# Performance work log

Measured on AMD Instinct MI355X. Metric: run time of the kernel, lower is better.

## Reference

```python
import jax, jax.numpy as jnp
import numpy as np

HIDDEN = 128
INPUT_DIM = 1
NUM_CLASSES = 2


def setup_inputs() -> dict:
    key = jax.random.key(0)
    ks = jax.random.split(key, 7)
    B, T = 256, 1024
    s_ih = 1.0 / np.sqrt(HIDDEN)
    x = jax.random.normal(ks[0], (B, T, INPUT_DIM), dtype=jnp.float32)
    W_ih = jax.random.uniform(ks[1], (HIDDEN, INPUT_DIM), jnp.float32, -s_ih, s_ih)
    W_hh = jax.random.uniform(ks[2], (HIDDEN, HIDDEN), jnp.float32, -s_ih, s_ih)
    b_ih = jax.random.uniform(ks[3], (HIDDEN,), jnp.float32, -s_ih, s_ih)
    b_hh = jax.random.uniform(ks[4], (HIDDEN,), jnp.float32, -s_ih, s_ih)
    W_fc = jax.random.uniform(ks[5], (NUM_CLASSES, HIDDEN), jnp.float32, -s_ih, s_ih)
    b_fc = jax.random.uniform(ks[6], (NUM_CLASSES,), jnp.float32, -s_ih, s_ih)
    return {"x": x, "W_ih": W_ih, "W_hh": W_hh, "b_ih": b_ih,
            "b_hh": b_hh, "W_fc": W_fc, "b_fc": b_fc}


def reference(x, W_ih, W_hh, b_ih, b_hh, W_fc, b_fc):
    B = x.shape[0]
    # Precompute input projection for all timesteps: [B,T,H]
    xp = jnp.einsum('bti,hi->bth', x, W_ih) + b_ih + b_hh
    h0 = jnp.zeros((B, HIDDEN), dtype=x.dtype)

    def step(h, xp_t):
        h_new = jnp.tanh(xp_t + h @ W_hh.T)  # [B,H]
        return h_new, h_new

    _, hs = jax.lax.scan(step, h0, jnp.swapaxes(xp, 0, 1))  # hs: [T,B,H]
    out = jnp.swapaxes(hs, 0, 1)  # [B,T,H]
    logits = jnp.einsum('bth,ch->btc', out, W_fc) + b_fc  # [B,T,C]
    return logits
```

## Files before the change

### kernel.cpp

```cpp
#include <hip/hip_runtime.h>

typedef float f32x2 __attribute__((ext_vector_type(2)));
typedef float f32x4 __attribute__((ext_vector_type(4)));

#define BB 256
#define TT 1024
#define HH 128
#define CC 2

#define LOG2E2 2.885390081777927f

__device__ __forceinline__ float ftanh2(float u2) {
    float e = __builtin_amdgcn_exp2f(u2);
    float r = __builtin_amdgcn_rcpf(e + 1.0f);
    return fmaf(-2.0f, r, 1.0f);
}

__device__ __forceinline__ float bcast(float v, int j) {
    return __int_as_float(__builtin_amdgcn_readlane(__float_as_int(v), j));
}

#define DPP_ADD(v, ctrl)                                                     \
    ((v) + __int_as_float(__builtin_amdgcn_mov_dpp(                          \
         __float_as_int(v), (ctrl), 0xF, 0xF, true)))

#define SYNC() asm volatile("s_waitcnt lgkmcnt(0)\n\ts_barrier" ::: "memory")

__global__ __launch_bounds__(256, 1) void rnn_kernel(
    const float* __restrict__ x, const float* __restrict__ W_ih,
    const float* __restrict__ W_hh, const float* __restrict__ b_ih,
    const float* __restrict__ b_hh, const float* __restrict__ W_fc,
    const float* __restrict__ b_fc, float* __restrict__ out)
{
    const int b   = blockIdx.x;
    const int tid = threadIdx.x;
    const int l   = tid & 63;
    const int wv  = tid >> 6;
    const int lq  = l & 31;
    const int kb  = wv << 5;
    const int rA  = l, rB = l + 64;
    const int rF  = kb + lq;

    __shared__ float xs[TT + 8];
    __shared__ f32x2 p2[2][4][64];
    __shared__ f32x2 qp[4][4];
    __shared__ f32x2 obuf[16];

    {
        const f32x4* xr = (const f32x4*)(x + (size_t)b * TT);
        ((f32x4*)xs)[tid] = xr[tid];
    }
    if (tid < 8) xs[TT + tid] = 0.f;

    const float wih  = W_ih[rF] * LOG2E2;
    const float bias = (b_ih[rF] + b_hh[rF]) * LOG2E2;
    const float wfs  = (l < 32) ? W_fc[rF] : W_fc[HH + rF];
    const float bf0  = b_fc[0], bf1 = b_fc[1];

    float wa[32], wb[32];
    {
        const f32x4* a4 = (const f32x4*)(W_hh + (size_t)rA * HH + kb);
        const f32x4* b4 = (const f32x4*)(W_hh + (size_t)rB * HH + kb);
        #pragma unroll
        for (int j = 0; j < 8; ++j) {
            f32x4 va = a4[j], vb = b4[j];
            wa[4*j+0] = va.x * LOG2E2; wa[4*j+1] = va.y * LOG2E2;
            wa[4*j+2] = va.z * LOG2E2; wa[4*j+3] = va.w * LOG2E2;
            wb[4*j+0] = vb.x * LOG2E2; wb[4*j+1] = vb.y * LOG2E2;
            wb[4*j+2] = vb.z * LOG2E2; wb[4*j+3] = vb.w * LOG2E2;
        }
    }

    float hn = 0.f;
    float* o = out + (size_t)b * TT * CC;

    __syncthreads();
    float xcur = xs[0];

    #pragma unroll 4
    for (int t = 0; t < TT; ++t) {
        const int buf = t & 1, qb = t & 3;

        #pragma unroll
        for (int k = 0; k < 32; ++k)
            asm volatile("" : "+v"(wa[k]), "+v"(wb[k]));

        float aA0 = 0.f, aA1 = 0.f, aB0 = 0.f, aB1 = 0.f;
        #pragma unroll
        for (int k = 0; k < 32; k += 2) {
            float s0 = bcast(hn, k);
            float s1 = bcast(hn, k + 1);
            aA0 = fmaf(wa[k],     s0, aA0);
            aB0 = fmaf(wb[k],     s0, aB0);
            aA1 = fmaf(wa[k + 1], s1, aA1);
            aB1 = fmaf(wb[k + 1], s1, aB1);
        }
        p2[buf][wv][l] = f32x2{ aA0 + aA1, aB0 + aB1 };
        const float xnext = xs[t + 1];

        SYNC();

        const float* pf = (const float*)&p2[buf][0][0]
                        + ((((wv & 1) << 5) + lq) << 1) + (wv >> 1);
        float p0 = pf[0], p1 = pf[128], pv2 = pf[256], pv3 = pf[384];

        {
            float q = wfs * hn;
            q = DPP_ADD(q, 0xB1);
            q = DPP_ADD(q, 0x4E);
            q = DPP_ADD(q, 0x124);
            q = DPP_ADD(q, 0x128);
            float q0 = bcast(q, 0)  + bcast(q, 16);
            float q1 = bcast(q, 32) + bcast(q, 48);
            if (l == 0) qp[qb][wv] = f32x2{q0, q1};
        }
        if (t >= 2 && tid == 0) {
            const int pq = (t - 1) & 3;
            f32x2 s = (qp[pq][0] + qp[pq][1]) + (qp[pq][2] + qp[pq][3]);
            s.x += bf0; s.y += bf1;
            obuf[(t - 2) & 15] = s;
        }
        if ((t & 15) == 1 && t >= 17 && tid < 32) {
            ((float*)(o + (t - 17) * CC))[tid] = ((const float*)obuf)[tid];
        }

        const float base = fmaf(xcur, wih, bias);
        xcur = xnext;
        hn = ftanh2(base + ((p0 + p1) + (pv2 + pv3)));
    }

    {
        float q = wfs * hn;
        q = DPP_ADD(q, 0xB1);
        q = DPP_ADD(q, 0x4E);
        q = DPP_ADD(q, 0x124);
        q = DPP_ADD(q, 0x128);
        float q0 = bcast(q, 0)  + bcast(q, 16);
        float q1 = bcast(q, 32) + bcast(q, 48);
        if (l == 0) qp[0][wv] = f32x2{q0, q1};
    }
    __syncthreads();
    if (tid == 0) {
        f32x2 s = (qp[3][0] + qp[3][1]) + (qp[3][2] + qp[3][3]);
        s.x += bf0; s.y += bf1;
        *(f32x2*)(o + (TT - 2) * CC) = s;
        f32x2 s2 = (qp[0][0] + qp[0][1]) + (qp[0][2] + qp[0][3]);
        s2.x += bf0; s2.y += bf1;
        *(f32x2*)(o + (TT - 1) * CC) = s2;
    }
    if (tid < 28) {
        ((float*)(o + 1008 * CC))[tid] = ((const float*)obuf)[tid];
    }
}

extern "C" void kernel_launch(void* const* d_in, const int* in_sizes, int n_in,
                              void* d_out, int out_size, void* d_ws, size_t ws_size,
                              hipStream_t stream) {
    const float* x    = (const float*)d_in[0];
    const float* W_ih = (const float*)d_in[1];
    const float* W_hh = (const float*)d_in[2];
    const float* b_ih = (const float*)d_in[3];
    const float* b_hh = (const float*)d_in[4];
    const float* W_fc = (const float*)d_in[5];
    const float* b_fc = (const float*)d_in[6];
    float* out = (float*)d_out;

    rnn_kernel<<<BB, 256, 0, stream>>>(x, W_ih, W_hh, b_ih, b_hh, W_fc, b_fc, out);
}
```

Measured before the change: 538.2 us.

## Split recurrent matvec across eight waves instead of four per batch row

Each block now uses 512 threads (8 waves), and each wave handles a 16-wide slice of the hidden dimension instead of 32. This halves the per-step serial readlane/FMA chain per wave and the register footprint for W_hh. In exchange, the cross-wave reduction reads eight partials from LDS instead of four and the barrier has to synchronise twice as many waves. The asm register-pinning loop is also removed.

```diff
diff --git a/kernel.cpp b/kernel.cpp
--- a/kernel.cpp
+++ b/kernel.cpp
@@ -7,6 +7,7 @@
 #define TT 1024
 #define HH 128
 #define CC 2
+#define NW 8
 
 #define LOG2E2 2.885390081777927f
 
@@ -26,7 +27,7 @@
 
 #define SYNC() asm volatile("s_waitcnt lgkmcnt(0)\n\ts_barrier" ::: "memory")
 
-__global__ __launch_bounds__(256, 1) void rnn_kernel(
+__global__ __launch_bounds__(512, 1) void rnn_kernel(
     const float* __restrict__ x, const float* __restrict__ W_ih,
     const float* __restrict__ W_hh, const float* __restrict__ b_ih,
     const float* __restrict__ b_hh, const float* __restrict__ W_fc,
@@ -36,17 +37,16 @@
     const int tid = threadIdx.x;
     const int l   = tid & 63;
     const int wv  = tid >> 6;
-    const int lq  = l & 31;
-    const int kb  = wv << 5;
+    const int kb  = wv << 4;
     const int rA  = l, rB = l + 64;
-    const int rF  = kb + lq;
+    const int rF  = kb + (l & 15);
 
     __shared__ float xs[TT + 8];
-    __shared__ f32x2 p2[2][4][64];
-    __shared__ f32x2 qp[4][4];
+    __shared__ f32x2 p2[2][NW][64];
+    __shared__ f32x2 qp[4][NW];
     __shared__ f32x2 obuf[16];
 
-    {
+    if (tid < 256) {
         const f32x4* xr = (const f32x4*)(x + (size_t)b * TT);
         ((f32x4*)xs)[tid] = xr[tid];
     }
@@ -54,15 +54,15 @@
 
     const float wih  = W_ih[rF] * LOG2E2;
     const float bias = (b_ih[rF] + b_hh[rF]) * LOG2E2;
-    const float wfs  = (l < 32) ? W_fc[rF] : W_fc[HH + rF];
-    const float bf0  = b_fc[0], bf1 = b_fc[1];
+    const float wfs = (l < 16) ? W_fc[rF] : ((l < 32) ? W_fc[HH + rF] : 0.f);
+    const float bf0 = b_fc[0], bf1 = b_fc[1];
 
-    float wa[32], wb[32];
+    float wa[16], wb[16];
     {
         const f32x4* a4 = (const f32x4*)(W_hh + (size_t)rA * HH + kb);
         const f32x4* b4 = (const f32x4*)(W_hh + (size_t)rB * HH + kb);
         #pragma unroll
-        for (int j = 0; j < 8; ++j) {
+        for (int j = 0; j < 4; ++j) {
             f32x4 va = a4[j], vb = b4[j];
             wa[4*j+0] = va.x * LOG2E2; wa[4*j+1] = va.y * LOG2E2;
             wa[4*j+2] = va.z * LOG2E2; wa[4*j+3] = va.w * LOG2E2;
@@ -74,6 +74,9 @@
     float hn = 0.f;
     float* o = out + (size_t)b * TT * CC;
 
+    const int rm  = rF & 63;
+    const int sel = rF >> 6;
+
     __syncthreads();
     float xcur = xs[0];
 
@@ -81,13 +84,9 @@
     for (int t = 0; t < TT; ++t) {
         const int buf = t & 1, qb = t & 3;
 
-        #pragma unroll
-        for (int k = 0; k < 32; ++k)
-            asm volatile("" : "+v"(wa[k]), "+v"(wb[k]));
-
         float aA0 = 0.f, aA1 = 0.f, aB0 = 0.f, aB1 = 0.f;
         #pragma unroll
-        for (int k = 0; k < 32; k += 2) {
+        for (int k = 0; k < 16; k += 2) {
             float s0 = bcast(hn, k);
             float s1 = bcast(hn, k + 1);
             aA0 = fmaf(wa[k],     s0, aA0);
@@ -100,9 +99,9 @@
 
         SYNC();
 
-        const float* pf = (const float*)&p2[buf][0][0]
-                        + ((((wv & 1) << 5) + lq) << 1) + (wv >> 1);
-        float p0 = pf[0], p1 = pf[128], pv2 = pf[256], pv3 = pf[384];
+        const float* pf = (const float*)&p2[buf][0][0] + (rm << 1) + sel;
+        float p0 = pf[0],   p1 = pf[128], pv2 = pf[256], pv3 = pf[384];
+        float p4 = pf[512], p5 = pf[640], p6  = pf[768], p7  = pf[896];
 
         {
             float q = wfs * hn;
@@ -110,13 +109,14 @@
             q = DPP_ADD(q, 0x4E);
             q = DPP_ADD(q, 0x124);
             q = DPP_ADD(q, 0x128);
-            float q0 = bcast(q, 0)  + bcast(q, 16);
-            float q1 = bcast(q, 32) + bcast(q, 48);
+            float q0 = bcast(q, 0);
+            float q1 = bcast(q, 16);
             if (l == 0) qp[qb][wv] = f32x2{q0, q1};
         }
         if (t >= 2 && tid == 0) {
             const int pq = (t - 1) & 3;
-            f32x2 s = (qp[pq][0] + qp[pq][1]) + (qp[pq][2] + qp[pq][3]);
+            f32x2 s = ((qp[pq][0] + qp[pq][1]) + (qp[pq][2] + qp[pq][3]))
+                    + ((qp[pq][4] + qp[pq][5]) + (qp[pq][6] + qp[pq][7]));
             s.x += bf0; s.y += bf1;
             obuf[(t - 2) & 15] = s;
         }
@@ -126,7 +126,8 @@
 
         const float base = fmaf(xcur, wih, bias);
         xcur = xnext;
-        hn = ftanh2(base + ((p0 + p1) + (pv2 + pv3)));
+        hn = ftanh2(base + (((p0 + p1) + (pv2 + pv3))
+                          + ((p4 + p5) + (p6  + p7))));
     }
 
     {
@@ -135,16 +136,18 @@
         q = DPP_ADD(q, 0x4E);
         q = DPP_ADD(q, 0x124);
         q = DPP_ADD(q, 0x128);
-        float q0 = bcast(q, 0)  + bcast(q, 16);
-        float q1 = bcast(q, 32) + bcast(q, 48);
+        float q0 = bcast(q, 0);
+        float q1 = bcast(q, 16);
         if (l == 0) qp[0][wv] = f32x2{q0, q1};
     }
     __syncthreads();
     if (tid == 0) {
-        f32x2 s = (qp[3][0] + qp[3][1]) + (qp[3][2] + qp[3][3]);
+        f32x2 s = ((qp[3][0] + qp[3][1]) + (qp[3][2] + qp[3][3]))
+                + ((qp[3][4] + qp[3][5]) + (qp[3][6] + qp[3][7]));
         s.x += bf0; s.y += bf1;
         *(f32x2*)(o + (TT - 2) * CC) = s;
-        f32x2 s2 = (qp[0][0] + qp[0][1]) + (qp[0][2] + qp[0][3]);
+        f32x2 s2 = ((qp[0][0] + qp[0][1]) + (qp[0][2] + qp[0][3]))
+                 + ((qp[0][4] + qp[0][5]) + (qp[0][6] + qp[0][7]));
         s2.x += bf0; s2.y += bf1;
         *(f32x2*)(o + (TT - 1) * CC) = s2;
     }
@@ -165,5 +168,5 @@
     const float* b_fc = (const float*)d_in[6];
     float* out = (float*)d_out;
 
-    rnn_kernel<<<BB, 256, 0, stream>>>(x, W_ih, W_hh, b_ih, b_hh, W_fc, b_fc, out);
+    rnn_kernel<<<BB, 512, 0, stream>>>(x, W_ih, W_hh, b_ih, b_hh, W_fc, b_fc, out);
 }
```

After: 450.4 us. 16.3% less time.

## Process two batch rows per block to interleave independent recurrences

Applied to the files above, without the earlier changes.

Each block now advances two sequences at once, sharing the register-resident W_hh and one barrier per timestep for both. This is meant to hide the serial latency of the recurrence (readlane broadcasts, LDS reduction, barrier, tanh) by overlapping two independent chains. In exchange, the grid halves to 128 blocks, leaving half the CUs idle, and per-step instruction work per block doubles.

```diff
diff --git a/kernel.cpp b/kernel.cpp
--- a/kernel.cpp
+++ b/kernel.cpp
@@ -3,7 +3,7 @@
 typedef float f32x2 __attribute__((ext_vector_type(2)));
 typedef float f32x4 __attribute__((ext_vector_type(4)));
 
-#define BB 256
+#define BB 128
 #define TT 1024
 #define HH 128
 #define CC 2
@@ -32,7 +32,7 @@
     const float* __restrict__ b_hh, const float* __restrict__ W_fc,
     const float* __restrict__ b_fc, float* __restrict__ out)
 {
-    const int b   = blockIdx.x;
+    const int b0  = blockIdx.x * 2;
     const int tid = threadIdx.x;
     const int l   = tid & 63;
     const int wv  = tid >> 6;
@@ -41,16 +41,18 @@
     const int rA  = l, rB = l + 64;
     const int rF  = kb + lq;
 
-    __shared__ float xs[TT + 8];
-    __shared__ f32x2 p2[2][4][64];
-    __shared__ f32x2 qp[4][4];
-    __shared__ f32x2 obuf[16];
+    __shared__ float xs[2][TT + 8];
+    __shared__ f32x2 p2[2][2][4][64];
+    __shared__ f32x2 qp[4][2][4];
+    __shared__ f32x2 obuf[2][16];
 
     {
-        const f32x4* xr = (const f32x4*)(x + (size_t)b * TT);
-        ((f32x4*)xs)[tid] = xr[tid];
-    }
-    if (tid < 8) xs[TT + tid] = 0.f;
+        const f32x4* xr0 = (const f32x4*)(x + (size_t)b0 * TT);
+        const f32x4* xr1 = (const f32x4*)(x + (size_t)(b0 + 1) * TT);
+        ((f32x4*)xs[0])[tid] = xr0[tid];
+        ((f32x4*)xs[1])[tid] = xr1[tid];
+    }
+    if (tid < 8) { xs[0][TT + tid] = 0.f; xs[1][TT + tid] = 0.f; }
 
     const float wih  = W_ih[rF] * LOG2E2;
     const float bias = (b_ih[rF] + b_hh[rF]) * LOG2E2;
@@ -69,87 +71,135 @@
             wb[4*j+0] = vb.x * LOG2E2; wb[4*j+1] = vb.y * LOG2E2;
             wb[4*j+2] = vb.z * LOG2E2; wb[4*j+3] = vb.w * LOG2E2;
         }
-    }
-
-    float hn = 0.f;
-    float* o = out + (size_t)b * TT * CC;
-
-    __syncthreads();
-    float xcur = xs[0];
-
-    #pragma unroll 4
-    for (int t = 0; t < TT; ++t) {
-        const int buf = t & 1, qb = t & 3;
-
         #pragma unroll
         for (int k = 0; k < 32; ++k)
             asm volatile("" : "+v"(wa[k]), "+v"(wb[k]));
-
-        float aA0 = 0.f, aA1 = 0.f, aB0 = 0.f, aB1 = 0.f;
-        #pragma unroll
-        for (int k = 0; k < 32; k += 2) {
-            float s0 = bcast(hn, k);
-            float s1 = bcast(hn, k + 1);
-            aA0 = fmaf(wa[k],     s0, aA0);
-            aB0 = fmaf(wb[k],     s0, aB0);
-            aA1 = fmaf(wa[k + 1], s1, aA1);
-            aB1 = fmaf(wb[k + 1], s1, aB1);
-        }
-        p2[buf][wv][l] = f32x2{ aA0 + aA1, aB0 + aB1 };
-        const float xnext = xs[t + 1];
+    }
+
+    float hn0 = 0.f, hn1 = 0.f;
+    float* o0 = out + (size_t)b0 * TT * CC;
+    float* o1 = out + (size_t)(b0 + 1) * TT * CC;
+
+    __syncthreads();
+    float xc0 = xs[0][0], xc1 = xs[1][0];
+
+    #pragma unroll 2
+    for (int t = 0; t < TT; ++t) {
+        const int buf = t & 1, qb = t & 3;
+
+        {
+            float aA0 = 0.f, aA1 = 0.f, aB0 = 0.f, aB1 = 0.f;
+            #pragma unroll
+            for (int k = 0; k < 32; k += 2) {
+                float s0 = bcast(hn0, k);
+                float s1 = bcast(hn0, k + 1);
+                aA0 = fmaf(wa[k],     s0, aA0);
+                aB0 = fmaf(wb[k],     s0, aB0);
+                aA1 = fmaf(wa[k + 1], s1, aA1);
+                aB1 = fmaf(wb[k + 1], s1, aB1);
+            }
+            p2[buf][0][wv][l] = f32x2{ aA0 + aA1, aB0 + aB1 };
+        }
+        {
+            float cA0 = 0.f, cA1 = 0.f, cB0 = 0.f, cB1 = 0.f;
+            #pragma unroll
+            for (int k = 0; k < 32; k += 2) {
+                float s0 = bcast(hn1, k);
+                float s1 = bcast(hn1, k + 1);
+                cA0 = fmaf(wa[k],     s0, cA0);
+                cB0 = fmaf(wb[k],     s0, cB0);
+                cA1 = fmaf(wa[k + 1], s1, cA1);
+                cB1 = fmaf(wb[k + 1], s1, cB1);
+            }
+            p2[buf][1][wv][l] = f32x2{ cA0 + cA1, cB0 + cB1 };
+        }
+        const float xn0 = xs[0][t + 1];
+        const float xn1 = xs[1][t + 1];
 
         SYNC();
 
-        const float* pf = (const float*)&p2[buf][0][0]
-                        + ((((wv & 1) << 5) + lq) << 1) + (wv >> 1);
-        float p0 = pf[0], p1 = pf[128], pv2 = pf[256], pv3 = pf[384];
-
-        {
-            float q = wfs * hn;
+        const int fofs = ((((wv & 1) << 5) + lq) << 1) + (wv >> 1);
+        const float* pf0 = (const float*)&p2[buf][0][0][0] + fofs;
+        const float* pf1 = (const float*)&p2[buf][1][0][0] + fofs;
+        float p00 = pf0[0], p01 = pf0[128], p02 = pf0[256], p03 = pf0[384];
+        float p10 = pf1[0], p11 = pf1[128], p12 = pf1[256], p13 = pf1[384];
+
+        {
+            float q = wfs * hn0;
             q = DPP_ADD(q, 0xB1);
             q = DPP_ADD(q, 0x4E);
             q = DPP_ADD(q, 0x124);
             q = DPP_ADD(q, 0x128);
             float q0 = bcast(q, 0)  + bcast(q, 16);
             float q1 = bcast(q, 32) + bcast(q, 48);
-            if (l == 0) qp[qb][wv] = f32x2{q0, q1};
+            if (l == 0) qp[qb][0][wv] = f32x2{q0, q1};
+        }
+        {
+            float q = wfs * hn1;
+            q = DPP_ADD(q, 0xB1);
+            q = DPP_ADD(q, 0x4E);
+            q = DPP_ADD(q, 0x124);
+            q = DPP_ADD(q, 0x128);
+            float q0 = bcast(q, 0)  + bcast(q, 16);
+            float q1 = bcast(q, 32) + bcast(q, 48);
+            if (l == 0) qp[qb][1][wv] = f32x2{q0, q1};
         }
         if (t >= 2 && tid == 0) {
             const int pq = (t - 1) & 3;
-            f32x2 s = (qp[pq][0] + qp[pq][1]) + (qp[pq][2] + qp[pq][3]);
-            s.x += bf0; s.y += bf1;
-            obuf[(t - 2) & 15] = s;
-        }
-        if ((t & 15) == 1 && t >= 17 && tid < 32) {
-            ((float*)(o + (t - 17) * CC))[tid] = ((const float*)obuf)[tid];
-        }
-
-        const float base = fmaf(xcur, wih, bias);
-        xcur = xnext;
-        hn = ftanh2(base + ((p0 + p1) + (pv2 + pv3)));
+            f32x2 s0 = (qp[pq][0][0] + qp[pq][0][1]) + (qp[pq][0][2] + qp[pq][0][3]);
+            s0.x += bf0; s0.y += bf1;
+            obuf[0][(t - 2) & 15] = s0;
+            f32x2 s1 = (qp[pq][1][0] + qp[pq][1][1]) + (qp[pq][1][2] + qp[pq][1][3]);
+            s1.x += bf0; s1.y += bf1;
+            obuf[1][(t - 2) & 15] = s1;
+        }
+        if ((t & 15) == 1 && t >= 17 && tid < 64) {
+            const int bb = tid >> 5, ln = tid & 31;
+            float* oo = bb ? o1 : o0;
+            ((float*)(oo + (t - 17) * CC))[ln] = ((const float*)obuf[bb])[ln];
+        }
+
+        const float base0 = fmaf(xc0, wih, bias);
+        const float base1 = fmaf(xc1, wih, bias);
+        xc0 = xn0; xc1 = xn1;
+        hn0 = ftanh2(base0 + ((p00 + p01) + (p02 + p03)));
+        hn1 = ftanh2(base1 + ((p10 + p11) + (p12 + p13)));
     }
 
     {
-        float q = wfs * hn;
-        q = DPP_ADD(q, 0xB1);
-        q = DPP_ADD(q, 0x4E);
-        q = DPP_ADD(q, 0x124);
-        q = DPP_ADD(q, 0x128);
+        float q = wfs * hn0;
+        q = DPP_ADD(q, 0xB1); q = DPP_ADD(q, 0x4E);
+        q = DPP_ADD(q, 0x124); q = DPP_ADD(q, 0x128);
         float q0 = bcast(q, 0)  + bcast(q, 16);
         float q1 = bcast(q, 32) + bcast(q, 48);
-        if (l == 0) qp[0][wv] = f32x2{q0, q1};
+        if (l == 0) qp[0][0][wv] = f32x2{q0, q1};
+        float r = wfs * hn1;
+        r = DPP_ADD(r, 0xB1); r = DPP_ADD(r, 0x4E);
+        r = DPP_ADD(r, 0x124); r = DPP_ADD(r, 0x128);
+        float r0 = bcast(r, 0)  + bcast(r, 16);
+        float r1 = bcast(r, 32) + bcast(r, 48);
+        if (l == 0) qp[0][1][wv] = f32x2{r0, r1};
     }
     __syncthreads();
     if (tid == 0) {
-        f32x2 s = (qp[3][0] + qp[3][1]) + (qp[3][2] + qp[3][3]);
+        f32x2 s = (qp[3][0][0] + qp[3][0][1]) + (qp[3][0][2] + qp[3][0][3]);
         s.x += bf0; s.y += bf1;
-        *(f32x2*)(o + (TT - 2) * CC) = s;
-        f32x2 s2 = (qp[0][0] + qp[0][1]) + (qp[0][2] + qp[0][3]);
+        *(f32x2*)(o0 + (TT - 2) * CC) = s;
+        f32x2 s2 = (qp[0][0][0] + qp[0][0][1]) + (qp[0][0][2] + qp[0][0][3]);
         s2.x += bf0; s2.y += bf1;
-        *(f32x2*)(o + (TT - 1) * CC) = s2;
+        *(f32x2*)(o0 + (TT - 1) * CC) = s2;
+        f32x2 u = (qp[3][1][0] + qp[3][1][1]) + (qp[3][1][2] + qp[3][1][3]);
+        u.x += bf0; u.y += bf1;
+        *(f32x2*)(o1 + (TT - 2) * CC) = u;
+        f32x2 u2 = (qp[0][1][0] + qp[0][1][1]) + (qp[0][1][2] + qp[0][1][3]);
+        u2.x += bf0; u2.y += bf1;
+        *(f32x2*)(o1 + (TT - 1) * CC) = u2;
     }
     if (tid < 28) {
-        ((float*)(o + 1008 * CC))[tid] = ((const float*)obuf)[tid];
+        ((float*)(o0 + 1008 * CC))[tid] = ((const float*)obuf[0])[tid];
+    }
+    if (tid >= 32 && tid < 60) {
+        ((float*)(o1 + 1008 * CC))[tid - 32] = ((const float*)obuf[1])[tid - 32];
     }
 }
 
```

After: 701.0 us. +30.2%, slower.
